# Kernel tuning notes

Hardware: AMD Instinct MI355X
Metric: run time of the kernel (lower is better)

The kernel has to match this reference:

```python
import jax, jax.numpy as jnp
import numpy as np

MAX_WEIGHT = 10.0  # config.max_weight
EPS = 1e-8

BATCH = 2048
VOCAB = 256
SEQ_LEN = 64
NUM_DENDRITES = SEQ_LEN * VOCAB  # 16384


def setup_inputs() -> dict:
    key = jax.random.key(0)
    k1, k2 = jax.random.split(key)
    # binary dendrite activations in {0,1}, stored as float32 as in the torch module
    binary = jax.random.randint(k1, (BATCH, NUM_DENDRITES), 0, 2).astype(jnp.float32)
    # raw_weights ~ Uniform(-1, 1) per nn.init.uniform_
    raw_weights = jax.random.uniform(k2, (VOCAB, NUM_DENDRITES), dtype=jnp.float32,
                                     minval=-1.0, maxval=1.0)
    return {"binary": binary, "raw_weights": raw_weights}


def reference(binary, raw_weights):
    # bounded positive weights: max_weight * sigmoid(raw)
    w = MAX_WEIGHT * jax.nn.sigmoid(raw_weights)            # (vocab, D)
    log_w = jnp.log(jnp.clip(w, EPS))                       # (vocab, D)
    # masked log-sum: where binary==0 the torch code uses log(1)=0, then multiplies
    # by binary anyway, so it is exactly binary @ log_w.T
    log_sum = jnp.einsum('bd,vd->bv', binary, log_w)        # (batch, vocab)
    n_active = jnp.clip(jnp.sum(binary, axis=-1, keepdims=True), 1.0)  # (batch, 1)
    logits = jnp.exp(log_sum / n_active)                    # geometric mean of fired weights
    return logits
```

## Files before the change

kernel.cpp:

```cpp
#include <hip/hip_runtime.h>

#define BATCH 2048
#define VOCAB 256
#define KDIM 16384
#define BM 64
#define BK 32
#define S_SPLIT 8
#define KCHUNK (KDIM / S_SPLIT)
#define NT (KCHUNK / BK)
#define LN10 2.302585092994046f

typedef __attribute__((ext_vector_type(8))) short short8;
typedef __attribute__((ext_vector_type(4))) float f32x4;

#define FENCE asm volatile("" ::: "memory")

__device__ __forceinline__ unsigned short f2bf_rne(float f) {
  unsigned int u = __float_as_uint(f);
  u += 0x7fffu + ((u >> 16) & 1u);
  return (unsigned short)(u >> 16);
}
__device__ __forceinline__ unsigned int pack2(float lo, float hi) {
  return (__float_as_uint(lo) >> 16) | (__float_as_uint(hi) & 0xffff0000u);
}

__device__ __forceinline__ void async16(void* lds, const void* g) {
  __builtin_amdgcn_global_load_lds(
      (const __attribute__((address_space(1))) unsigned int*)g,
      (__attribute__((address_space(3))) unsigned int*)lds, 16, 0, 0);
}

__global__ __launch_bounds__(256) void k_logw(const float* __restrict__ raw,
                                              unsigned short* __restrict__ logw) {
  int i = blockIdx.x * 256 + threadIdx.x;
  float4 x = ((const float4*)raw)[i];
  ushort4 r;
  r.x = f2bf_rne(LN10 - log1pf(expf(-x.x)));
  r.y = f2bf_rne(LN10 - log1pf(expf(-x.y)));
  r.z = f2bf_rne(LN10 - log1pf(expf(-x.z)));
  r.w = f2bf_rne(LN10 - log1pf(expf(-x.w)));
  ((ushort4*)logw)[i] = r;
}

template <int PART>
__global__ __launch_bounds__(256) void k_gemm(
    const float* __restrict__ binary, const unsigned short* __restrict__ logw,
    float* __restrict__ outp, float* __restrict__ nactp) {
  __shared__ char smem[65536];
  char* const Bb0 = smem;
  char* const Bb1 = smem + 16384;
  char* const Bb2 = smem + 32768;
  char* const Bb3 = smem + 49152;

  const int tid = threadIdx.x;
  const int wv = tid >> 6;
  const int lane = tid & 63;
  const int l15 = lane & 15;
  const int lhi = lane >> 4;
  const int bx = blockIdx.x;
  const int by = blockIdx.y;
  const int phase = ((bx & 7) + by * 8) & (NT - 1);

  const float* asrc =
      binary + (size_t)(bx * BM + wv * 16 + l15) * KDIM + by * KCHUNK + lhi * 8;

  const int brow = lane >> 2;
  const int bslot = (lane & 3) ^ (brow & 3);
  const unsigned short* bsrc =
      logw + (size_t)(wv * 64 + brow) * KDIM + by * KCHUNK + bslot * 8;
  const int bdst = wv * 4096 + lane * 16;

  const int rdoff = l15 * 64 + ((lhi ^ (l15 & 3)) << 4);

  f32x4 acc[16];
#pragma unroll
  for (int n = 0; n < 16; ++n) acc[n] = f32x4{0.f, 0.f, 0.f, 0.f};
  float asum = 0.f;
  float4 A0[2], A1[2], A2[2], A3[2];

  auto STAGE = [&](int t, char* B, float4* A) {
    const int kk = ((t + phase) & (NT - 1)) * BK;
#pragma unroll
    for (int i = 0; i < 4; ++i)
      async16(B + bdst + i * 1024, bsrc + (size_t)i * 16 * KDIM + kk);
    const float4* p = (const float4*)(asrc + kk);
    A[0] = p[0];
    A[1] = p[1];
  };
  auto COMPUTE = [&](const char* B, const float4* A) {
    asum += A[0].x + A[0].y + A[0].z + A[0].w +
            A[1].x + A[1].y + A[1].z + A[1].w;
    union { short8 s; unsigned int u[4]; } af;
    af.u[0] = pack2(A[0].x, A[0].y);
    af.u[1] = pack2(A[0].z, A[0].w);
    af.u[2] = pack2(A[1].x, A[1].y);
    af.u[3] = pack2(A[1].z, A[1].w);
#pragma unroll
    for (int n = 0; n < 16; ++n) {
      short8 bf = *(const short8*)(B + n * 1024 + rdoff);
      acc[n] = __builtin_amdgcn_mfma_f32_16x16x32_bf16(bf, af.s, acc[n], 0, 0, 0);
    }
  };

#define BAR __builtin_amdgcn_s_barrier()
#define VMW(N) asm volatile("s_waitcnt vmcnt(" #N ")" ::: "memory")

  STAGE(0, Bb0, A0); FENCE;
  STAGE(1, Bb1, A1); FENCE;
  STAGE(2, Bb2, A2); FENCE;

#pragma unroll 1
  for (int t = 0; t < NT - 4; t += 4) {
    BAR; FENCE; STAGE(t + 3, Bb3, A3); FENCE; VMW(18); BAR; FENCE;
    COMPUTE(Bb0, A0); FENCE;
    BAR; FENCE; STAGE(t + 4, Bb0, A0); FENCE; VMW(18); BAR; FENCE;
    COMPUTE(Bb1, A1); FENCE;
    BAR; FENCE; STAGE(t + 5, Bb1, A1); FENCE; VMW(18); BAR; FENCE;
    COMPUTE(Bb2, A2); FENCE;
    BAR; FENCE; STAGE(t + 6, Bb2, A2); FENCE; VMW(18); BAR; FENCE;
    COMPUTE(Bb3, A3); FENCE;
  }
  BAR; FENCE; STAGE(NT - 1, Bb3, A3); FENCE; VMW(18); BAR; FENCE;
  COMPUTE(Bb0, A0); FENCE;
  BAR; FENCE; VMW(12); BAR; FENCE;
  COMPUTE(Bb1, A1); FENCE;
  BAR; FENCE; VMW(6); BAR; FENCE;
  COMPUTE(Bb2, A2); FENCE;
  BAR; FENCE; VMW(0); BAR; FENCE;
  COMPUTE(Bb3, A3); FENCE;

  float s = asum;
  s += __shfl_xor(s, 16, 64);
  s += __shfl_xor(s, 32, 64);
  const int row = bx * BM + wv * 16 + l15;

  if (PART) {
    if (lane < 16) nactp[by * BATCH + row] = s;
    float* dst = outp + ((size_t)by * BATCH + row) * VOCAB + lhi * 4;
#pragma unroll
    for (int n = 0; n < 16; ++n)
      *(float4*)(dst + n * 16) =
          (float4){acc[n][0], acc[n][1], acc[n][2], acc[n][3]};
  } else {
    if (lane < 16) atomicAdd(&nactp[row], s);
#pragma unroll
    for (int n = 0; n < 16; ++n)
#pragma unroll
      for (int i = 0; i < 4; ++i)
        atomicAdd(&outp[(size_t)row * VOCAB + n * 16 + lhi * 4 + i], acc[n][i]);
  }
}

__global__ __launch_bounds__(256) void k_reduce(const float* __restrict__ part,
                                                const float* __restrict__ nactp,
                                                float* __restrict__ out) {
  int b = blockIdx.x;
  int v = threadIdx.x;
  float sum = 0.f, n = 0.f;
#pragma unroll
  for (int i = 0; i < S_SPLIT; ++i) {
    sum += part[((size_t)i * BATCH + b) * VOCAB + v];
    n += nactp[i * BATCH + b];
  }
  out[(size_t)b * VOCAB + v] = expf(sum / fmaxf(n, 1.f));
}

__global__ __launch_bounds__(256) void k_out(float* __restrict__ io,
                                             const float* __restrict__ nact) {
  int b = blockIdx.x;
  int v = threadIdx.x;
  float n = fmaxf(nact[b], 1.0f);
  size_t idx = (size_t)b * VOCAB + v;
  io[idx] = expf(io[idx] / n);
}

extern "C" void kernel_launch(void* const* d_in, const int* in_sizes, int n_in,
                              void* d_out, int out_size, void* d_ws, size_t ws_size,
                              hipStream_t stream) {
  const float* binary = (const float*)d_in[0];
  const float* raw = (const float*)d_in[1];
  float* out = (float*)d_out;
  char* ws = (char*)d_ws;

  const size_t LOGW_B = (size_t)VOCAB * KDIM * 2;
  const size_t NACT_B = (size_t)S_SPLIT * BATCH * 4;
  const size_t PART_B = (size_t)S_SPLIT * BATCH * VOCAB * 4;
  unsigned short* logw = (unsigned short*)ws;
  float* nactp = (float*)(ws + LOGW_B);
  float* part = (float*)(ws + LOGW_B + NACT_B);

  k_logw<<<(VOCAB * KDIM / 4) / 256, 256, 0, stream>>>(raw, logw);

  dim3 g(BATCH / BM, S_SPLIT);
  if (ws_size >= LOGW_B + NACT_B + PART_B) {
    k_gemm<1><<<g, 256, 0, stream>>>(binary, logw, part, nactp);
    k_reduce<<<BATCH, VOCAB, 0, stream>>>(part, nactp, out);
  } else {
    hipMemsetAsync(out, 0, (size_t)BATCH * VOCAB * sizeof(float), stream);
    hipMemsetAsync(nactp, 0, BATCH * sizeof(float), stream);
    k_gemm<0><<<g, 256, 0, stream>>>(binary, logw, out, nactp);
    k_out<<<BATCH, VOCAB, 0, stream>>>(out, nactp);
  }
}
```

Before: 240.3 us.

## Restructure GEMM with 64x64 per-wave tiles, LDS-staged A and finer K split

Each wave now computes a 64x64 output tile (4x4 MFMAs) instead of 16x256. Both the binary activations (converted to bf16) and logw are staged through swizzled LDS, so B fragments are reused across four A tiles. The 4-deep async B ring becomes a single buffer with a register double-buffered A prefetch. BK rises to 64 and S_SPLIT to 32, with a swapped grid order and launch bounds asking for 3 blocks per CU. The aim is more operand reuse per LDS read and higher occupancy, at the cost of a much larger partial-sum buffer and heavier reduce traffic, plus less latency hiding from the single B buffer.

```diff
diff --git a/kernel.cpp b/kernel.cpp
--- a/kernel.cpp
+++ b/kernel.cpp
@@ -4,8 +4,8 @@
 #define VOCAB 256
 #define KDIM 16384
 #define BM 64
-#define BK 32
-#define S_SPLIT 8
+#define BK 64
+#define S_SPLIT 32
 #define KCHUNK (KDIM / S_SPLIT)
 #define NT (KCHUNK / BK)
 #define LN10 2.302585092994046f
@@ -43,111 +43,130 @@
 }
 
 template <int PART>
-__global__ __launch_bounds__(256) void k_gemm(
+__global__ __launch_bounds__(256, 3) void k_gemm(
     const float* __restrict__ binary, const unsigned short* __restrict__ logw,
     float* __restrict__ outp, float* __restrict__ nactp) {
-  __shared__ char smem[65536];
-  char* const Bb0 = smem;
-  char* const Bb1 = smem + 16384;
-  char* const Bb2 = smem + 32768;
-  char* const Bb3 = smem + 49152;
+  __shared__ char smem[40960];
+  char* const Asm = smem;
+  char* const Bsm = smem + 8192;
 
   const int tid = threadIdx.x;
   const int wv = tid >> 6;
   const int lane = tid & 63;
   const int l15 = lane & 15;
   const int lhi = lane >> 4;
-  const int bx = blockIdx.x;
-  const int by = blockIdx.y;
-  const int phase = ((bx & 7) + by * 8) & (NT - 1);
-
-  const float* asrc =
-      binary + (size_t)(bx * BM + wv * 16 + l15) * KDIM + by * KCHUNK + lhi * 8;
-
-  const int brow = lane >> 2;
-  const int bslot = (lane & 3) ^ (brow & 3);
+  const int sx = blockIdx.x;
+  const int my = blockIdx.y;
+  const int m0 = my * BM;
+  const int k0 = sx * KCHUNK;
+
+  const int ar = tid >> 2, ac = tid & 3;
+  const float* asrc = binary + (size_t)(m0 + ar) * KDIM + k0 + ac * 16;
+  const int ar7 = ar & 7;
+  const int aw0 = ar * 128 + ((((ac * 2) ^ ar7) << 4));
+  const int aw1 = ar * 128 + ((((ac * 2 + 1) ^ ar7) << 4));
+
   const unsigned short* bsrc =
-      logw + (size_t)(wv * 64 + brow) * KDIM + by * KCHUNK + bslot * 8;
-  const int bdst = wv * 4096 + lane * 16;
-
-  const int rdoff = l15 * 64 + ((lhi ^ (l15 & 3)) << 4);
-
-  f32x4 acc[16];
-#pragma unroll
-  for (int n = 0; n < 16; ++n) acc[n] = f32x4{0.f, 0.f, 0.f, 0.f};
+      logw + (size_t)(wv * 64 + (lane >> 3)) * KDIM + k0 +
+      (((lane & 7) ^ (lane >> 3)) << 3);
+
+  const int rsw = (l15 & 7) << 4;
+
+  f32x4 acc[4][4];
+#pragma unroll
+  for (int m = 0; m < 4; ++m)
+#pragma unroll
+    for (int n = 0; n < 4; ++n) acc[m][n] = f32x4{0.f, 0.f, 0.f, 0.f};
   float asum = 0.f;
-  float4 A0[2], A1[2], A2[2], A3[2];
-
-  auto STAGE = [&](int t, char* B, float4* A) {
-    const int kk = ((t + phase) & (NT - 1)) * BK;
-#pragma unroll
-    for (int i = 0; i < 4; ++i)
-      async16(B + bdst + i * 1024, bsrc + (size_t)i * 16 * KDIM + kk);
-    const float4* p = (const float4*)(asrc + kk);
-    A[0] = p[0];
-    A[1] = p[1];
-  };
-  auto COMPUTE = [&](const char* B, const float4* A) {
-    asum += A[0].x + A[0].y + A[0].z + A[0].w +
-            A[1].x + A[1].y + A[1].z + A[1].w;
-    union { short8 s; unsigned int u[4]; } af;
-    af.u[0] = pack2(A[0].x, A[0].y);
-    af.u[1] = pack2(A[0].z, A[0].w);
-    af.u[2] = pack2(A[1].x, A[1].y);
-    af.u[3] = pack2(A[1].z, A[1].w);
-#pragma unroll
-    for (int n = 0; n < 16; ++n) {
-      short8 bf = *(const short8*)(B + n * 1024 + rdoff);
-      acc[n] = __builtin_amdgcn_mfma_f32_16x16x32_bf16(bf, af.s, acc[n], 0, 0, 0);
+  float4 Ra[4], Rb[4];
+
+  auto ALOAD = [&](int t, float4* R) {
+    const float4* p = (const float4*)(asrc + t * BK);
+    R[0] = p[0]; R[1] = p[1]; R[2] = p[2]; R[3] = p[3];
+  };
+  auto BSTAGE = [&](int t) {
+#pragma unroll
+    for (int i = 0; i < 8; ++i)
+      async16(Bsm + (wv * 64 + i * 8) * 128, bsrc + (size_t)i * 8 * KDIM + t * BK);
+  };
+  auto AWRITE = [&](const float4* R) {
+#pragma unroll
+    for (int j = 0; j < 4; ++j)
+      asum += R[j].x + R[j].y + R[j].z + R[j].w;
+    uint4 u0, u1;
+    u0.x = pack2(R[0].x, R[0].y); u0.y = pack2(R[0].z, R[0].w);
+    u0.z = pack2(R[1].x, R[1].y); u0.w = pack2(R[1].z, R[1].w);
+    u1.x = pack2(R[2].x, R[2].y); u1.y = pack2(R[2].z, R[2].w);
+    u1.z = pack2(R[3].x, R[3].y); u1.w = pack2(R[3].z, R[3].w);
+    *(uint4*)(Asm + aw0) = u0;
+    *(uint4*)(Asm + aw1) = u1;
+  };
+  auto COMPUTE = [&]() {
+#pragma unroll
+    for (int ks = 0; ks < 2; ++ks) {
+      const int koff = ((ks * 64) | (lhi * 16)) ^ rsw;
+      short8 af[4], bf[4];
+#pragma unroll
+      for (int m = 0; m < 4; ++m)
+        af[m] = *(const short8*)(Asm + (m * 16 + l15) * 128 + koff);
+#pragma unroll
+      for (int n = 0; n < 4; ++n)
+        bf[n] = *(const short8*)(Bsm + (wv * 64 + n * 16 + l15) * 128 + koff);
+#pragma unroll
+      for (int m = 0; m < 4; ++m)
+#pragma unroll
+        for (int n = 0; n < 4; ++n)
+          acc[m][n] = __builtin_amdgcn_mfma_f32_16x16x32_bf16(bf[n], af[m],
+                                                              acc[m][n], 0, 0, 0);
     }
   };
 
+#define VMW4 asm volatile("s_waitcnt vmcnt(4) lgkmcnt(0)" ::: "memory")
 #define BAR __builtin_amdgcn_s_barrier()
-#define VMW(N) asm volatile("s_waitcnt vmcnt(" #N ")" ::: "memory")
-
-  STAGE(0, Bb0, A0); FENCE;
-  STAGE(1, Bb1, A1); FENCE;
-  STAGE(2, Bb2, A2); FENCE;
-
+
+  ALOAD(0, Ra);
 #pragma unroll 1
-  for (int t = 0; t < NT - 4; t += 4) {
-    BAR; FENCE; STAGE(t + 3, Bb3, A3); FENCE; VMW(18); BAR; FENCE;
-    COMPUTE(Bb0, A0); FENCE;
-    BAR; FENCE; STAGE(t + 4, Bb0, A0); FENCE; VMW(18); BAR; FENCE;
-    COMPUTE(Bb1, A1); FENCE;
-    BAR; FENCE; STAGE(t + 5, Bb1, A1); FENCE; VMW(18); BAR; FENCE;
-    COMPUTE(Bb2, A2); FENCE;
-    BAR; FENCE; STAGE(t + 6, Bb2, A2); FENCE; VMW(18); BAR; FENCE;
-    COMPUTE(Bb3, A3); FENCE;
-  }
-  BAR; FENCE; STAGE(NT - 1, Bb3, A3); FENCE; VMW(18); BAR; FENCE;
-  COMPUTE(Bb0, A0); FENCE;
-  BAR; FENCE; VMW(12); BAR; FENCE;
-  COMPUTE(Bb1, A1); FENCE;
-  BAR; FENCE; VMW(6); BAR; FENCE;
-  COMPUTE(Bb2, A2); FENCE;
-  BAR; FENCE; VMW(0); BAR; FENCE;
-  COMPUTE(Bb3, A3); FENCE;
+  for (int t = 0; t < NT; t += 2) {
+    BSTAGE(t);
+    AWRITE(Ra);
+    ALOAD(t + 1, Rb);
+    VMW4; BAR; FENCE;
+    COMPUTE();
+    FENCE; BAR; FENCE;
+    BSTAGE(t + 1);
+    AWRITE(Rb);
+    ALOAD(t + 2 < NT ? t + 2 : NT - 1, Ra);
+    VMW4; BAR; FENCE;
+    COMPUTE();
+    FENCE; BAR; FENCE;
+  }
 
   float s = asum;
-  s += __shfl_xor(s, 16, 64);
-  s += __shfl_xor(s, 32, 64);
-  const int row = bx * BM + wv * 16 + l15;
+  s += __shfl_xor(s, 1, 64);
+  s += __shfl_xor(s, 2, 64);
 
   if (PART) {
-    if (lane < 16) nactp[by * BATCH + row] = s;
-    float* dst = outp + ((size_t)by * BATCH + row) * VOCAB + lhi * 4;
-#pragma unroll
-    for (int n = 0; n < 16; ++n)
-      *(float4*)(dst + n * 16) =
-          (float4){acc[n][0], acc[n][1], acc[n][2], acc[n][3]};
+    if (ac == 0) nactp[sx * BATCH + m0 + ar] = s;
+#pragma unroll
+    for (int m = 0; m < 4; ++m) {
+      float* dst = outp + ((size_t)sx * BATCH + m0 + m * 16 + l15) * VOCAB +
+                   wv * 64 + lhi * 4;
+#pragma unroll
+      for (int n = 0; n < 4; ++n)
+        *(float4*)(dst + n * 16) =
+            (float4){acc[m][n][0], acc[m][n][1], acc[m][n][2], acc[m][n][3]};
+    }
   } else {
-    if (lane < 16) atomicAdd(&nactp[row], s);
-#pragma unroll
-    for (int n = 0; n < 16; ++n)
-#pragma unroll
-      for (int i = 0; i < 4; ++i)
-        atomicAdd(&outp[(size_t)row * VOCAB + n * 16 + lhi * 4 + i], acc[n][i]);
+    if (ac == 0) atomicAdd(&nactp[m0 + ar], s);
+#pragma unroll
+    for (int m = 0; m < 4; ++m)
+#pragma unroll
+      for (int n = 0; n < 4; ++n)
+#pragma unroll
+        for (int i = 0; i < 4; ++i)
+          atomicAdd(&outp[(size_t)(m0 + m * 16 + l15) * VOCAB + wv * 64 +
+                          n * 16 + lhi * 4 + i],
+                    acc[m][n][i]);
   }
 }
 
@@ -191,7 +210,7 @@
 
   k_logw<<<(VOCAB * KDIM / 4) / 256, 256, 0, stream>>>(raw, logw);
 
-  dim3 g(BATCH / BM, S_SPLIT);
+  dim3 g(S_SPLIT, BATCH / BM);
   if (ws_size >= LOGW_B + NACT_B + PART_B) {
     k_gemm<1><<<g, 256, 0, stream>>>(binary, logw, part, nactp);
     k_reduce<<<BATCH, VOCAB, 0, stream>>>(part, nactp, out);
```

New measurement: 262.7 us. 9.3% more time.
